# Kernel tuning notes

Hardware: AMD Instinct MI355X
Metric: run time of the kernel (lower is better)

## Reference

```python
import jax, jax.numpy as jnp
import numpy as np


def _l2_normalize(x, eps=1e-12):
    # matches torch.nn.functional.normalize(p=2, dim=-1)
    n = jnp.linalg.norm(x, axis=-1, keepdims=True)
    return x / jnp.maximum(n, eps)


def setup_inputs() -> dict:
    key = jax.random.key(0)
    kq, kk, kv = jax.random.split(key, 3)
    B, H, N, D = 4, 12, 8192, 64
    Q = jax.random.normal(kq, (B, H, N, D), dtype=jnp.float32)
    K = jax.random.normal(kk, (B, H, N, D), dtype=jnp.float32)
    V = jax.random.normal(kv, (B, H, N, D), dtype=jnp.float32)
    mask = jnp.ones((B, N), dtype=jnp.float32)
    return {"Q": Q, "K": K, "V": V, "mask": mask}


def reference(Q, K, V, mask):
    N = Q.shape[2]
    scale = 1.0 / np.sqrt(np.sqrt(N)).astype(np.float32)  # N^{-1/4}
    m = mask[:, None, :, None]                 # [B,1,N,1]
    Qf = _l2_normalize(Q) * scale              # [B,H,N,D]
    Kf = _l2_normalize(K) * m * scale          # [B,H,N,D]
    Vm = V * m                                 # [B,H,N,D]
    # linear attention: (K^T V) is [B,H,D,D], then Q @ (K^T V)
    KtV = jnp.einsum('bhnd,bhne->bhde', Kf, Vm)
    return jnp.einsum('bhnd,bhde->bhne', Qf, KtV)
```

## Files before the change

kernel.cpp:

```cpp
#include <hip/hip_runtime.h>
#include <cmath>

#define Bn 4
#define Hn 12
#define BH 48
#define Nn 8192
#define Dn 64

typedef float f32x4 __attribute__((ext_vector_type(4)));
typedef short bf16x8 __attribute__((ext_vector_type(8)));

__device__ __forceinline__ int swz(int d) { return ((d >> 2) & 7) << 3; }

__device__ __forceinline__ unsigned cvt_pk_bf16(float lo, float hi) {
    unsigned r;
    asm("v_cvt_pk_bf16_f32 %0, %1, %2" : "=v"(r) : "v"(lo), "v"(hi));
    return r;
}

__global__ __launch_bounds__(256) void ktv_kernel(
    const float* __restrict__ K, const float* __restrict__ V,
    const float* __restrict__ mask, float* __restrict__ partial,
    float scale, int ch)
{
    const int chunk = blockIdx.x, head = blockIdx.y;
    const int bb = head / Hn;
    const int rowsPer = Nn / ch;
    const int n0 = chunk * rowsPer;
    const float* Kp = K + ((size_t)head * Nn + n0) * Dn;
    const float* Vp = V + ((size_t)head * Nn + n0) * Dn;
    const float* mp = mask + (size_t)bb * Nn + n0;

    __shared__ __align__(16) ushort sKT[64 * 64];
    __shared__ __align__(16) ushort sVT[64 * 64];

    const int t = threadIdx.x;
    const int w = t >> 6, l = t & 63;
    const int g = t >> 4;
    const int c4 = (t & 15) << 2;

    f32x4 acc[4] = {{0.f,0.f,0.f,0.f},{0.f,0.f,0.f,0.f},
                    {0.f,0.f,0.f,0.f},{0.f,0.f,0.f,0.f}};

    float4 kr[4], vr[4];
    float mk[4];
    #pragma unroll
    for (int s = 0; s < 4; ++s) {
        kr[s] = *(const float4*)(Kp + (size_t)(4*g + s) * Dn + c4);
        vr[s] = *(const float4*)(Vp + (size_t)(4*g + s) * Dn + c4);
        mk[s] = mp[4*g + s];
    }

    const int ntiles = rowsPer >> 6;
    for (int tt = 0; tt < ntiles; ++tt) {
        float rf[4];
        #pragma unroll
        for (int s = 0; s < 4; ++s) {
            float ss = kr[s].x*kr[s].x + kr[s].y*kr[s].y
                     + kr[s].z*kr[s].z + kr[s].w*kr[s].w;
            #pragma unroll
            for (int off = 1; off < 16; off <<= 1) ss += __shfl_xor(ss, off, 64);
            rf[s] = scale * mk[s] * mk[s] / fmaxf(sqrtf(ss), 1e-12f);
        }

        __syncthreads();
        const float* krf = (const float*)kr;
        const float* vrf = (const float*)vr;
        #pragma unroll
        for (int j = 0; j < 4; ++j) {
            const int d = c4 + j;
            const int base = d * 64;
            const int sw = swz(d);
            const int p0 = (4*g)     ^ sw;
            const int p2 = (4*g + 2) ^ sw;
            *(unsigned*)&sKT[base + p0] = cvt_pk_bf16(krf[j]     * rf[0], krf[4+j]  * rf[1]);
            *(unsigned*)&sKT[base + p2] = cvt_pk_bf16(krf[8+j]   * rf[2], krf[12+j] * rf[3]);
            *(unsigned*)&sVT[base + p0] = cvt_pk_bf16(vrf[j],            vrf[4+j]);
            *(unsigned*)&sVT[base + p2] = cvt_pk_bf16(vrf[8+j],          vrf[12+j]);
        }
        __syncthreads();

        if (tt + 1 < ntiles) {
            const float* Kn = Kp + (size_t)(tt + 1) * 64 * Dn;
            const float* Vn = Vp + (size_t)(tt + 1) * 64 * Dn;
            #pragma unroll
            for (int s = 0; s < 4; ++s) {
                kr[s] = *(const float4*)(Kn + (size_t)(4*g + s) * Dn + c4);
                vr[s] = *(const float4*)(Vn + (size_t)(4*g + s) * Dn + c4);
                mk[s] = mp[(tt + 1) * 64 + 4*g + s];
            }
        }

        const int e   = (w << 4) + (l & 15);
        const int nsl = (l >> 4) << 3;
        const int swe = swz(e);
        #pragma unroll
        for (int h = 0; h < 2; ++h) {
            const bf16x8 a = *(const bf16x8*)&sVT[e * 64 + ((h*32 + nsl) ^ swe)];
            #pragma unroll
            for (int P = 0; P < 4; ++P) {
                const int d = (P << 4) + (l & 15);
                const bf16x8 bq = *(const bf16x8*)&sKT[d * 64 + ((h*32 + nsl) ^ swz(d))];
                acc[P] = __builtin_amdgcn_mfma_f32_16x16x32_bf16(a, bq, acc[P], 0, 0, 0);
            }
        }
    }

    float* pp = partial + (size_t)(head * ch + chunk) * (Dn * Dn);
    #pragma unroll
    for (int P = 0; P < 4; ++P)
        #pragma unroll
        for (int r = 0; r < 4; ++r)
            pp[((w << 4) + ((l >> 4) << 2) + r) * 64 + (P << 4) + (l & 15)] = acc[P][r];
}

__global__ __launch_bounds__(256) void ktv_reduce_kernel(
    const float* __restrict__ partial, ushort* __restrict__ ktvT, int ch)
{
    const int head = blockIdx.y;
    const int e = blockIdx.x * 256 + threadIdx.x;
    const float* pp = partial + (size_t)head * ch * (Dn * Dn) + e;
    float s = 0.f;
    for (int c = 0; c < ch; ++c) s += pp[(size_t)c * (Dn * Dn)];
    unsigned u = __float_as_uint(s);
    u = (u + 0x7fffu + ((u >> 16) & 1u)) >> 16;
    ktvT[(size_t)head * (Dn * Dn) + e] = (ushort)u;
}

__global__ __launch_bounds__(256) void qktv_kernel(
    const float* __restrict__ Q, const ushort* __restrict__ ktvT,
    float* __restrict__ out, float scale)
{
    const int chunk = blockIdx.x, head = blockIdx.y;
    const int n0 = chunk * (Nn / 16);
    const float* Qp = Q + ((size_t)head * Nn + n0) * Dn;
    float* Op = out + ((size_t)head * Nn + n0) * Dn;
    const ushort* kp = ktvT + (size_t)head * (Dn * Dn);

    const int t = threadIdx.x, w = t >> 6, l = t & 63;
    const int lr = l & 15;
    const int lg = l >> 4;

    bf16x8 bf[4][2];
    #pragma unroll
    for (int E = 0; E < 4; ++E)
        #pragma unroll
        for (int h = 0; h < 2; ++h)
            bf[E][h] = *(const bf16x8*)&kp[(16*E + lr) * 64 + 32*h + 8*lg];

    for (int i = 0; i < 8; ++i) {
        const int strip = i * 4 + w;
        const float* qrow = Qp + (size_t)(strip * 16 + lr) * Dn;
        const float4 f0 = *(const float4*)(qrow + 8*lg);
        const float4 f1 = *(const float4*)(qrow + 8*lg + 4);
        const float4 f2 = *(const float4*)(qrow + 32 + 8*lg);
        const float4 f3 = *(const float4*)(qrow + 32 + 8*lg + 4);

        float ss = f0.x*f0.x + f0.y*f0.y + f0.z*f0.z + f0.w*f0.w
                 + f1.x*f1.x + f1.y*f1.y + f1.z*f1.z + f1.w*f1.w
                 + f2.x*f2.x + f2.y*f2.y + f2.z*f2.z + f2.w*f2.w
                 + f3.x*f3.x + f3.y*f3.y + f3.z*f3.z + f3.w*f3.w;
        ss += __shfl_xor(ss, 16, 64);
        ss += __shfl_xor(ss, 32, 64);
        const float inv = scale / fmaxf(sqrtf(ss), 1e-12f);

        union { unsigned u[4]; bf16x8 v; } a0, a1;
        a0.u[0] = cvt_pk_bf16(f0.x*inv, f0.y*inv);
        a0.u[1] = cvt_pk_bf16(f0.z*inv, f0.w*inv);
        a0.u[2] = cvt_pk_bf16(f1.x*inv, f1.y*inv);
        a0.u[3] = cvt_pk_bf16(f1.z*inv, f1.w*inv);
        a1.u[0] = cvt_pk_bf16(f2.x*inv, f2.y*inv);
        a1.u[1] = cvt_pk_bf16(f2.z*inv, f2.w*inv);
        a1.u[2] = cvt_pk_bf16(f3.x*inv, f3.y*inv);
        a1.u[3] = cvt_pk_bf16(f3.z*inv, f3.w*inv);

        #pragma unroll
        for (int E = 0; E < 4; ++E) {
            f32x4 c = {0.f, 0.f, 0.f, 0.f};
            c = __builtin_amdgcn_mfma_f32_16x16x32_bf16(a0.v, bf[E][0], c, 0, 0, 0);
            c = __builtin_amdgcn_mfma_f32_16x16x32_bf16(a1.v, bf[E][1], c, 0, 0, 0);
            #pragma unroll
            for (int r = 0; r < 4; ++r)
                Op[(size_t)(strip * 16 + 4*lg + r) * Dn + 16*E + lr] = c[r];
        }
    }
}

extern "C" void kernel_launch(void* const* d_in, const int* in_sizes, int n_in,
                              void* d_out, int out_size, void* d_ws, size_t ws_size,
                              hipStream_t stream)
{
    const float* Q    = (const float*)d_in[0];
    const float* K    = (const float*)d_in[1];
    const float* V    = (const float*)d_in[2];
    const float* mask = (const float*)d_in[3];
    float* out = (float*)d_out;

    const float scale = 1.0f / sqrtf(sqrtf((float)Nn));

    const size_t KTV_BYTES = (size_t)BH * Dn * Dn * sizeof(ushort);
    int ch = 16;
    while (ch > 1 &&
           KTV_BYTES + (size_t)BH * ch * Dn * Dn * 4 > ws_size)
        ch >>= 1;

    ushort* ktvT   = (ushort*)d_ws;
    float* partial = (float*)((char*)d_ws + KTV_BYTES);

    ktv_kernel<<<dim3(ch, BH), 256, 0, stream>>>(K, V, mask, partial, scale, ch);
    ktv_reduce_kernel<<<dim3((Dn * Dn) / 256, BH), 256, 0, stream>>>(partial, ktvT, ch);
    qktv_kernel<<<dim3(16, BH), 256, 0, stream>>>(Q, ktvT, out, scale);
}
```

Baseline: 100.6 us.

## Give each wave a private KtV tile loop without block barriers, reduce via LDS

```diff
diff --git a/kernel.cpp b/kernel.cpp
--- a/kernel.cpp
+++ b/kernel.cpp
@@ -10,15 +10,15 @@
 typedef float f32x4 __attribute__((ext_vector_type(4)));
 typedef short bf16x8 __attribute__((ext_vector_type(8)));
 
-__device__ __forceinline__ int swz(int d) { return ((d >> 2) & 7) << 3; }
-
 __device__ __forceinline__ unsigned cvt_pk_bf16(float lo, float hi) {
     unsigned r;
     asm("v_cvt_pk_bf16_f32 %0, %1, %2" : "=v"(r) : "v"(lo), "v"(hi));
     return r;
 }
 
-__global__ __launch_bounds__(256) void ktv_kernel(
+union F16 { float4 v[4]; float f[16]; };
+
+__global__ __launch_bounds__(256, 3) void ktv_kernel(
     const float* __restrict__ K, const float* __restrict__ V,
     const float* __restrict__ mask, float* __restrict__ partial,
     float scale, int ch)
@@ -26,92 +26,117 @@
     const int chunk = blockIdx.x, head = blockIdx.y;
     const int bb = head / Hn;
     const int rowsPer = Nn / ch;
-    const int n0 = chunk * rowsPer;
-    const float* Kp = K + ((size_t)head * Nn + n0) * Dn;
-    const float* Vp = V + ((size_t)head * Nn + n0) * Dn;
-    const float* mp = mask + (size_t)bb * Nn + n0;
-
-    __shared__ __align__(16) ushort sKT[64 * 64];
-    __shared__ __align__(16) ushort sVT[64 * 64];
+    const int waveRows = rowsPer >> 2;
 
     const int t = threadIdx.x;
     const int w = t >> 6, l = t & 63;
-    const int g = t >> 4;
-    const int c4 = (t & 15) << 2;
-
-    f32x4 acc[4] = {{0.f,0.f,0.f,0.f},{0.f,0.f,0.f,0.f},
-                    {0.f,0.f,0.f,0.f},{0.f,0.f,0.f,0.f}};
-
-    float4 kr[4], vr[4];
-    float mk[4];
-    #pragma unroll
-    for (int s = 0; s < 4; ++s) {
-        kr[s] = *(const float4*)(Kp + (size_t)(4*g + s) * Dn + c4);
-        vr[s] = *(const float4*)(Vp + (size_t)(4*g + s) * Dn + c4);
-        mk[s] = mp[4*g + s];
-    }
-
-    const int ntiles = rowsPer >> 6;
-    for (int tt = 0; tt < ntiles; ++tt) {
-        float rf[4];
-        #pragma unroll
-        for (int s = 0; s < 4; ++s) {
-            float ss = kr[s].x*kr[s].x + kr[s].y*kr[s].y
-                     + kr[s].z*kr[s].z + kr[s].w*kr[s].w;
-            #pragma unroll
-            for (int off = 1; off < 16; off <<= 1) ss += __shfl_xor(ss, off, 64);
-            rf[s] = scale * mk[s] * mk[s] / fmaxf(sqrtf(ss), 1e-12f);
-        }
-
+    const int p = l & 15, q = l >> 4;
+    const int gq = q << 3;
+
+    const size_t base = ((size_t)head * Nn + (size_t)chunk * rowsPer + (size_t)w * waveRows) * Dn;
+    const float* Kp = K + base;
+    const float* Vp = V + base;
+    const float* mp = mask + (size_t)bb * Nn + (size_t)chunk * rowsPer + (size_t)w * waveRows;
+
+    __shared__ __align__(16) ushort S[16384];
+    ushort* sKT = S + w * 4096;
+    ushort* sVT = sKT + 2048;
+
+    f32x4 acc[4][4];
+    #pragma unroll
+    for (int a = 0; a < 4; ++a)
+        #pragma unroll
+        for (int b2 = 0; b2 < 4; ++b2) acc[a][b2] = (f32x4){0.f, 0.f, 0.f, 0.f};
+
+    const int r0 = 2 * p, r1 = r0 + 1;
+    const int cb = 16 * q;
+
+    F16 ka, kb, va, vb;
+    float m0, m1;
+    #pragma unroll
+    for (int i = 0; i < 4; ++i) {
+        ka.v[i] = *(const float4*)(Kp + (size_t)r0 * Dn + cb + 4 * i);
+        kb.v[i] = *(const float4*)(Kp + (size_t)r1 * Dn + cb + 4 * i);
+        va.v[i] = *(const float4*)(Vp + (size_t)r0 * Dn + cb + 4 * i);
+        vb.v[i] = *(const float4*)(Vp + (size_t)r1 * Dn + cb + 4 * i);
+    }
+    m0 = mp[r0]; m1 = mp[r1];
+
+    const int nt = waveRows >> 5;
+    for (int c = 0; c < nt; ++c) {
+        float ss0 = 0.f, ss1 = 0.f;
+        #pragma unroll
+        for (int i = 0; i < 16; ++i) { ss0 += ka.f[i] * ka.f[i]; ss1 += kb.f[i] * kb.f[i]; }
+        ss0 += __shfl_xor(ss0, 16, 64); ss0 += __shfl_xor(ss0, 32, 64);
+        ss1 += __shfl_xor(ss1, 16, 64); ss1 += __shfl_xor(ss1, 32, 64);
+        const float rf0 = scale * m0 * m0 / fmaxf(sqrtf(ss0), 1e-12f);
+        const float rf1 = scale * m1 * m1 / fmaxf(sqrtf(ss1), 1e-12f);
+
+        const int np = r0 ^ gq;
+        #pragma unroll
+        for (int j = 0; j < 16; ++j)
+            *(unsigned*)&sVT[(cb + j) * 32 + np] = cvt_pk_bf16(va.f[j], vb.f[j]);
+        #pragma unroll
+        for (int j = 0; j < 16; ++j)
+            *(unsigned*)&sKT[(cb + j) * 32 + np] = cvt_pk_bf16(ka.f[j] * rf0, kb.f[j] * rf1);
+
+        if (c + 1 < nt) {
+            const float* Kn = Kp + (size_t)(c + 1) * 32 * Dn;
+            #pragma unroll
+            for (int i = 0; i < 4; ++i) {
+                ka.v[i] = *(const float4*)(Kn + (size_t)r0 * Dn + cb + 4 * i);
+                kb.v[i] = *(const float4*)(Kn + (size_t)r1 * Dn + cb + 4 * i);
+            }
+            m0 = mp[(c + 1) * 32 + r0]; m1 = mp[(c + 1) * 32 + r1];
+        }
+
+        bf16x8 af[4], bfr[4];
+        #pragma unroll
+        for (int tj = 0; tj < 4; ++tj)
+            af[tj] = *(const bf16x8*)&sVT[(16 * tj + p) * 32 + ((8 * q) ^ (tj << 3))];
+        #pragma unroll
+        for (int P = 0; P < 4; ++P)
+            bfr[P] = *(const bf16x8*)&sKT[(16 * P + p) * 32 + ((8 * q) ^ (P << 3))];
+        #pragma unroll
+        for (int tj = 0; tj < 4; ++tj)
+            #pragma unroll
+            for (int P = 0; P < 4; ++P)
+                acc[tj][P] = __builtin_amdgcn_mfma_f32_16x16x32_bf16(af[tj], bfr[P], acc[tj][P], 0, 0, 0);
+
+        if (c + 1 < nt) {
+            const float* Vn = Vp + (size_t)(c + 1) * 32 * Dn;
+            #pragma unroll
+            for (int i = 0; i < 4; ++i) {
+                va.v[i] = *(const float4*)(Vn + (size_t)r0 * Dn + cb + 4 * i);
+                vb.v[i] = *(const float4*)(Vn + (size_t)r1 * Dn + cb + 4 * i);
+            }
+        }
+    }
+
+    __syncthreads();
+    float* sAcc = (float*)S;
+    #pragma unroll
+    for (int ww = 0; ww < 4; ++ww) {
+        if (w == ww) {
+            #pragma unroll
+            for (int tj = 0; tj < 4; ++tj)
+                #pragma unroll
+                for (int P = 0; P < 4; ++P)
+                    #pragma unroll
+                    for (int r = 0; r < 4; ++r) {
+                        float* ptr = &sAcc[(16 * tj + 4 * q + r) * 64 + 16 * P + p];
+                        *ptr = (ww == 0) ? acc[tj][P][r] : (*ptr + acc[tj][P][r]);
+                    }
+        }
         __syncthreads();
-        const float* krf = (const float*)kr;
-        const float* vrf = (const float*)vr;
-        #pragma unroll
-        for (int j = 0; j < 4; ++j) {
-            const int d = c4 + j;
-            const int base = d * 64;
-            const int sw = swz(d);
-            const int p0 = (4*g)     ^ sw;
-            const int p2 = (4*g + 2) ^ sw;
-            *(unsigned*)&sKT[base + p0] = cvt_pk_bf16(krf[j]     * rf[0], krf[4+j]  * rf[1]);
-            *(unsigned*)&sKT[base + p2] = cvt_pk_bf16(krf[8+j]   * rf[2], krf[12+j] * rf[3]);
-            *(unsigned*)&sVT[base + p0] = cvt_pk_bf16(vrf[j],            vrf[4+j]);
-            *(unsigned*)&sVT[base + p2] = cvt_pk_bf16(vrf[8+j],          vrf[12+j]);
-        }
-        __syncthreads();
-
-        if (tt + 1 < ntiles) {
-            const float* Kn = Kp + (size_t)(tt + 1) * 64 * Dn;
-            const float* Vn = Vp + (size_t)(tt + 1) * 64 * Dn;
-            #pragma unroll
-            for (int s = 0; s < 4; ++s) {
-                kr[s] = *(const float4*)(Kn + (size_t)(4*g + s) * Dn + c4);
-                vr[s] = *(const float4*)(Vn + (size_t)(4*g + s) * Dn + c4);
-                mk[s] = mp[(tt + 1) * 64 + 4*g + s];
-            }
-        }
-
-        const int e   = (w << 4) + (l & 15);
-        const int nsl = (l >> 4) << 3;
-        const int swe = swz(e);
-        #pragma unroll
-        for (int h = 0; h < 2; ++h) {
-            const bf16x8 a = *(const bf16x8*)&sVT[e * 64 + ((h*32 + nsl) ^ swe)];
-            #pragma unroll
-            for (int P = 0; P < 4; ++P) {
-                const int d = (P << 4) + (l & 15);
-                const bf16x8 bq = *(const bf16x8*)&sKT[d * 64 + ((h*32 + nsl) ^ swz(d))];
-                acc[P] = __builtin_amdgcn_mfma_f32_16x16x32_bf16(a, bq, acc[P], 0, 0, 0);
-            }
-        }
     }
 
     float* pp = partial + (size_t)(head * ch + chunk) * (Dn * Dn);
     #pragma unroll
-    for (int P = 0; P < 4; ++P)
-        #pragma unroll
-        for (int r = 0; r < 4; ++r)
-            pp[((w << 4) + ((l >> 4) << 2) + r) * 64 + (P << 4) + (l & 15)] = acc[P][r];
+    for (int u = 0; u < 4; ++u) {
+        const int f = t + u * 256;
+        *(float4*)(pp + 4 * f) = *(const float4*)(sAcc + 4 * f);
+    }
 }
 
 __global__ __launch_bounds__(256) void ktv_reduce_kernel(
@@ -146,15 +171,15 @@
     for (int E = 0; E < 4; ++E)
         #pragma unroll
         for (int h = 0; h < 2; ++h)
-            bf[E][h] = *(const bf16x8*)&kp[(16*E + lr) * 64 + 32*h + 8*lg];
+            bf[E][h] = *(const bf16x8*)&kp[(16 * E + lr) * 64 + 32 * h + 8 * lg];
 
     for (int i = 0; i < 8; ++i) {
         const int strip = i * 4 + w;
         const float* qrow = Qp + (size_t)(strip * 16 + lr) * Dn;
-        const float4 f0 = *(const float4*)(qrow + 8*lg);
-        const float4 f1 = *(const float4*)(qrow + 8*lg + 4);
-        const float4 f2 = *(const float4*)(qrow + 32 + 8*lg);
-        const float4 f3 = *(const float4*)(qrow + 32 + 8*lg + 4);
+        const float4 f0 = *(const float4*)(qrow + 8 * lg);
+        const float4 f1 = *(const float4*)(qrow + 8 * lg + 4);
+        const float4 f2 = *(const float4*)(qrow + 32 + 8 * lg);
+        const float4 f3 = *(const float4*)(qrow + 32 + 8 * lg + 4);
 
         float ss = f0.x*f0.x + f0.y*f0.y + f0.z*f0.z + f0.w*f0.w
                  + f1.x*f1.x + f1.y*f1.y + f1.z*f1.z + f1.w*f1.w
@@ -176,12 +201,12 @@
 
         #pragma unroll
         for (int E = 0; E < 4; ++E) {
-            f32x4 c = {0.f, 0.f, 0.f, 0.f};
-            c = __builtin_amdgcn_mfma_f32_16x16x32_bf16(a0.v, bf[E][0], c, 0, 0, 0);
-            c = __builtin_amdgcn_mfma_f32_16x16x32_bf16(a1.v, bf[E][1], c, 0, 0, 0);
+            f32x4 cacc = {0.f, 0.f, 0.f, 0.f};
+            cacc = __builtin_amdgcn_mfma_f32_16x16x32_bf16(a0.v, bf[E][0], cacc, 0, 0, 0);
+            cacc = __builtin_amdgcn_mfma_f32_16x16x32_bf16(a1.v, bf[E][1], cacc, 0, 0, 0);
             #pragma unroll
             for (int r = 0; r < 4; ++r)
-                Op[(size_t)(strip * 16 + 4*lg + r) * Dn + 16*E + lr] = c[r];
+                Op[(size_t)(strip * 16 + 4 * lg + r) * Dn + 16 * E + lr] = cacc[r];
         }
     }
 }
@@ -199,9 +224,8 @@
     const float scale = 1.0f / sqrtf(sqrtf((float)Nn));
 
     const size_t KTV_BYTES = (size_t)BH * Dn * Dn * sizeof(ushort);
-    int ch = 16;
-    while (ch > 1 &&
-           KTV_BYTES + (size_t)BH * ch * Dn * Dn * 4 > ws_size)
+    int ch = 32;
+    while (ch > 1 && KTV_BYTES + (size_t)BH * ch * Dn * Dn * 4 > ws_size)
         ch >>= 1;
 
     ushort* ktvT   = (ushort*)d_ws;
```

After: 116.6 us. 15.9% more time.
